# Optimization experiments

Hardware: AMD Instinct MI355X
Metric: run time of the kernel (lower is better)

## Reference

```python
import jax, jax.numpy as jnp
import numpy as np

N = 8192
IN_DIM = 256
OUT_DIM = 256  # out_dim//num_heads * num_heads == out_dim
EDGE_PROB = 0.01


def setup_inputs() -> dict:
    key = jax.random.key(0)
    k_adj, k_h, k_q, k_k, k_v = jax.random.split(key, 5)
    # Dense 0/1 adjacency mask, multiplied into the score matrix.
    adj = (jax.random.uniform(k_adj, (N, N)) < EDGE_PROB).astype(jnp.float32)
    h = jax.random.normal(k_h, (N, IN_DIM), dtype=jnp.float32)
    # torch nn.Linear stores weight as [out_features, in_features]; no bias (use_bias=False).
    s = 1.0 / np.sqrt(IN_DIM)
    Wq = jax.random.normal(k_q, (OUT_DIM, IN_DIM), dtype=jnp.float32) * s
    Wk = jax.random.normal(k_k, (OUT_DIM, IN_DIM), dtype=jnp.float32) * s
    Wv = jax.random.normal(k_v, (OUT_DIM, IN_DIM), dtype=jnp.float32) * s
    return {"adj": adj, "h": h, "Wq": Wq, "Wk": Wk, "Wv": Wv}


def reference(adj, h, Wq, Wk, Wv):
    # Q_h, K_h, V_h: [N, out_dim]
    Q_h = h @ Wq.T
    K_h = h @ Wk.T
    V_h = h @ Wv.T
    scale = 1.0 / jnp.sqrt(jnp.asarray(h.shape[1], dtype=h.dtype))
    # Scores masked multiplicatively by adjacency (faithful to source: zeros,
    # not -inf, so non-edges still contribute exp(0) after softmax).
    A_tilde = scale * (Q_h @ K_h.T) * adj            # [N, N]
    attention = jax.nn.softmax(A_tilde, axis=1)       # softmax over dim 1
    X_tilde = attention @ V_h                         # [N, out_dim]
    return X_tilde
```

## Files before the change

kernel.cpp:

```cpp
#include <hip/hip_runtime.h>


#define NN  8192
#define DIM 256
#define SCALE 0.0625f
#define CAP 128

typedef __attribute__((ext_vector_type(8))) short short8;
typedef __attribute__((ext_vector_type(4))) float f32x4;
typedef __attribute__((ext_vector_type(4))) unsigned int u32x4;

__device__ __forceinline__ unsigned short f2bf(float f) {
    union { float f; unsigned u; } v; v.f = f;
    unsigned u = v.u;
    unsigned r = (u + 0x7fffu + ((u >> 16) & 1u)) >> 16;
    return (unsigned short)r;
}
__device__ __forceinline__ float bf2f(unsigned short s) {
    union { unsigned u; float f; } v; v.u = ((unsigned)s) << 16;
    return v.f;
}
__device__ __forceinline__ float dw_lo(unsigned u) {
    union { unsigned u; float f; } v; v.u = u << 16; return v.f;
}
__device__ __forceinline__ float dw_hi(unsigned u) {
    union { unsigned u; float f; } v; v.u = u & 0xffff0000u; return v.f;
}

__global__ __launch_bounds__(256) void prep_kernel(
    const float* __restrict__ h, const float* __restrict__ Wq,
    const float* __restrict__ Wk, const float* __restrict__ Wv,
    unsigned short* __restrict__ h_bf, unsigned short* __restrict__ w_bf)
{
    int b = blockIdx.x, t = threadIdx.x;
    if (b < 2048) {
        int idx = (b * 256 + t) * 4;
        float4 v = *(const float4*)(h + idx);
        ushort4 o; o.x = f2bf(v.x); o.y = f2bf(v.y); o.z = f2bf(v.z); o.w = f2bf(v.w);
        *(ushort4*)(h_bf + idx) = o;
    } else {
        int idx = ((b - 2048) * 256 + t) * 4;
        int w = idx >> 16;
        int offn = idx & 65535;
        const float* src = (w == 0) ? Wq : (w == 1) ? Wk : Wv;
        float4 v = *(const float4*)(src + offn);
        ushort4 o; o.x = f2bf(v.x); o.y = f2bf(v.y); o.z = f2bf(v.z); o.w = f2bf(v.w);
        *(ushort4*)(w_bf + idx) = o;
    }
}

__global__ __launch_bounds__(256) void proj_gemm(
    const unsigned short* __restrict__ h_bf, const unsigned short* __restrict__ w_bf,
    float* __restrict__ Q, unsigned short* __restrict__ Kb, unsigned short* __restrict__ Vb)
{
    __shared__ unsigned short sB[256][40];
    const int mb = blockIdx.x, p = blockIdx.y;
    const unsigned short* W = w_bf + (p << 16);
    const int tid = threadIdx.x, wave = tid >> 6, lane = tid & 63;

    f32x4 acc[16];
#pragma unroll
    for (int f = 0; f < 16; ++f) acc[f] = (f32x4)(0.0f);

    const int arow = mb * 64 + wave * 16 + (lane & 15);
    const int ko   = (lane >> 4) * 8;

    for (int kk = 0; kk < 256; kk += 32) {
        __syncthreads();
        {
            const uint4* src = (const uint4*)(W + tid * 256 + kk);
            uint4* dst = (uint4*)(&sB[tid][0]);
            dst[0] = src[0]; dst[1] = src[1]; dst[2] = src[2]; dst[3] = src[3];
        }
        __syncthreads();
        short8 a = *(const short8*)(h_bf + (size_t)arow * 256 + kk + ko);
#pragma unroll
        for (int f = 0; f < 16; ++f) {
            short8 b = *(const short8*)(&sB[f * 16 + (lane & 15)][ko]);
            acc[f] = __builtin_amdgcn_mfma_f32_16x16x32_bf16(a, b, acc[f], 0, 0, 0);
        }
    }

    const int orow = mb * 64 + wave * 16 + ((lane >> 4) << 2);
    const int ocol = lane & 15;
    if (p == 0) {
#pragma unroll
        for (int f = 0; f < 16; ++f)
#pragma unroll
            for (int r = 0; r < 4; ++r)
                Q[(size_t)(orow + r) * 256 + f * 16 + ocol] = acc[f][r];
    } else {
        unsigned short* dstb = (p == 1) ? Kb : Vb;
#pragma unroll
        for (int f = 0; f < 16; ++f)
#pragma unroll
            for (int r = 0; r < 4; ++r)
                dstb[(size_t)(orow + r) * 256 + f * 16 + ocol] = f2bf(acc[f][r]);
    }
}

__global__ __launch_bounds__(256) void vsum_partial(
    const unsigned short* __restrict__ Vb, float* __restrict__ partial)
{
    int b = blockIdx.x, t = threadIdx.x;
    float s = 0.0f;
    for (int r = 0; r < 64; ++r)
        s += bf2f(Vb[(size_t)(b * 64 + r) * 256 + t]);
    partial[b * 256 + t] = s;
}
__global__ __launch_bounds__(256) void vsum_final(
    const float* __restrict__ partial, float* __restrict__ Vsum)
{
    int t = threadIdx.x;
    float s = 0.0f;
    for (int b = 0; b < 128; ++b) s += partial[b * 256 + t];
    Vsum[t] = s;
}

__global__ __launch_bounds__(256) void attn_main(
    const float* __restrict__ adj, const float* __restrict__ Q,
    const unsigned short* __restrict__ Kb, const unsigned short* __restrict__ Vb,
    const float* __restrict__ Vsum, float* __restrict__ out)
{
    __shared__ int   s_idx[4][CAP];
    __shared__ float s_acc[4][256];
    __shared__ float s_den[4];

    const int i    = blockIdx.x;
    const int tid  = threadIdx.x;
    const int lane = tid & 63;
    const int wave = tid >> 6;

    const f32x4* arow = (const f32x4*)(adj + (size_t)i * NN);
    f32x4 av[8];
#pragma unroll
    for (int it = 0; it < 8; ++it)
        av[it] = __builtin_nontemporal_load(arow + (wave * 512 + it * 64 + lane));

    const unsigned long long lt = (1ull << lane) - 1ull;
    int off = 0;
#pragma unroll
    for (int it = 0; it < 8; ++it) {
        const int colbase = (wave * 512 + it * 64 + lane) * 4;
#pragma unroll
        for (int c = 0; c < 4; ++c) {
            bool nz = (av[it][c] != 0.0f);
            unsigned long long m = __ballot(nz);
            if (nz) s_idx[wave][off + __popcll(m & lt)] = colbase + c;
            off += __popcll(m);
        }
    }

    const float* Qi = Q + (size_t)i * DIM + (lane & 15) * 16;
    f32x4 q0 = *(const f32x4*)(Qi);
    f32x4 q1 = *(const f32x4*)(Qi + 4);
    f32x4 q2 = *(const f32x4*)(Qi + 8);
    f32x4 q3 = *(const f32x4*)(Qi + 12);

    const int g = lane >> 4;
    float acc0 = 0.f, acc1 = 0.f, acc2 = 0.f, acc3 = 0.f, den = 0.f;
    const int rounds = (off + 3) >> 2;

#pragma unroll 2
    for (int r = 0; r < rounds; ++r) {
        const int kb0 = r * 4;
        int jg0 = (kb0 + 0 < off) ? s_idx[wave][kb0 + 0] : 0;
        int jg1 = (kb0 + 1 < off) ? s_idx[wave][kb0 + 1] : 0;
        int jg2 = (kb0 + 2 < off) ? s_idx[wave][kb0 + 2] : 0;
        int jg3 = (kb0 + 3 < off) ? s_idx[wave][kb0 + 3] : 0;

        const bool myv = (kb0 + g) < off;
        const int  myj = (g == 0) ? jg0 : (g == 1) ? jg1 : (g == 2) ? jg2 : jg3;

        const u32x4* kp = (const u32x4*)(Kb + (size_t)myj * DIM + (lane & 15) * 16);
        u32x4 ka = kp[0];
        u32x4 kc = kp[1];

        ushort4 v0 = *(const ushort4*)(Vb + (size_t)jg0 * DIM + lane * 4);
        ushort4 v1 = *(const ushort4*)(Vb + (size_t)jg1 * DIM + lane * 4);
        ushort4 v2 = *(const ushort4*)(Vb + (size_t)jg2 * DIM + lane * 4);
        ushort4 v3 = *(const ushort4*)(Vb + (size_t)jg3 * DIM + lane * 4);

        float d0 = q0[0] * dw_lo(ka[0]);
        float d1 = q0[1] * dw_hi(ka[0]);
        float d2 = q0[2] * dw_lo(ka[1]);
        float d3 = q0[3] * dw_hi(ka[1]);
        d0 = fmaf(q1[0], dw_lo(ka[2]), d0);
        d1 = fmaf(q1[1], dw_hi(ka[2]), d1);
        d2 = fmaf(q1[2], dw_lo(ka[3]), d2);
        d3 = fmaf(q1[3], dw_hi(ka[3]), d3);
        d0 = fmaf(q2[0], dw_lo(kc[0]), d0);
        d1 = fmaf(q2[1], dw_hi(kc[0]), d1);
        d2 = fmaf(q2[2], dw_lo(kc[1]), d2);
        d3 = fmaf(q2[3], dw_hi(kc[1]), d3);
        d0 = fmaf(q3[0], dw_lo(kc[2]), d0);
        d1 = fmaf(q3[1], dw_hi(kc[2]), d1);
        d2 = fmaf(q3[2], dw_lo(kc[3]), d2);
        d3 = fmaf(q3[3], dw_hi(kc[3]), d3);
        float d = (d0 + d1) + (d2 + d3);

        d += __shfl_xor(d, 1);
        d += __shfl_xor(d, 2);
        d += __shfl_xor(d, 4);
        d += __shfl_xor(d, 8);

        float e = myv ? (__expf(SCALE * d) - 1.0f) : 0.0f;

        float e0 = __shfl(e, 0);
        float e1 = __shfl(e, 16);
        float e2 = __shfl(e, 32);
        float e3 = __shfl(e, 48);
        den += (e0 + e1) + (e2 + e3);

        acc0 = fmaf(e0, bf2f(v0.x), acc0); acc1 = fmaf(e0, bf2f(v0.y), acc1);
        acc2 = fmaf(e0, bf2f(v0.z), acc2); acc3 = fmaf(e0, bf2f(v0.w), acc3);
        acc0 = fmaf(e1, bf2f(v1.x), acc0); acc1 = fmaf(e1, bf2f(v1.y), acc1);
        acc2 = fmaf(e1, bf2f(v1.z), acc2); acc3 = fmaf(e1, bf2f(v1.w), acc3);
        acc0 = fmaf(e2, bf2f(v2.x), acc0); acc1 = fmaf(e2, bf2f(v2.y), acc1);
        acc2 = fmaf(e2, bf2f(v2.z), acc2); acc3 = fmaf(e2, bf2f(v2.w), acc3);
        acc0 = fmaf(e3, bf2f(v3.x), acc0); acc1 = fmaf(e3, bf2f(v3.y), acc1);
        acc2 = fmaf(e3, bf2f(v3.z), acc2); acc3 = fmaf(e3, bf2f(v3.w), acc3);
    }

    f32x4 accv = {acc0, acc1, acc2, acc3};
    *(f32x4*)(&s_acc[wave][lane * 4]) = accv;
    if (lane == 0) s_den[wave] = den;
    __syncthreads();

    float a = (s_acc[0][tid] + s_acc[1][tid]) + (s_acc[2][tid] + s_acc[3][tid]);
    float dn = (s_den[0] + s_den[1]) + (s_den[2] + s_den[3]);
    out[(size_t)i * DIM + tid] = (Vsum[tid] + a) / (8192.0f + dn);
}

extern "C" void kernel_launch(void* const* d_in, const int* in_sizes, int n_in,
                              void* d_out, int out_size, void* d_ws, size_t ws_size,
                              hipStream_t stream)
{
    const float* adj = (const float*)d_in[0];
    const float* h   = (const float*)d_in[1];
    const float* Wq  = (const float*)d_in[2];
    const float* Wk  = (const float*)d_in[3];
    const float* Wv  = (const float*)d_in[4];
    float* out = (float*)d_out;

    char* ws = (char*)d_ws;
    size_t off = 0;
    unsigned short* p_hbf = (unsigned short*)(ws + off); off += (size_t)NN * DIM * 2;
    unsigned short* p_wbf = (unsigned short*)(ws + off); off += (size_t)3 * DIM * DIM * 2;
    off = (off + 1023) & ~(size_t)1023;
    float*          p_Q   = (float*)(ws + off);          off += (size_t)NN * DIM * 4;
    unsigned short* p_Kb  = (unsigned short*)(ws + off); off += (size_t)NN * DIM * 2;
    unsigned short* p_Vb  = (unsigned short*)(ws + off); off += (size_t)NN * DIM * 2;
    float*          p_par = (float*)(ws + off);          off += (size_t)128 * DIM * 4;
    float*          p_vs  = (float*)(ws + off);          off += DIM * 4;
    (void)ws_size; (void)in_sizes; (void)n_in; (void)out_size;

    prep_kernel<<<2240, 256, 0, stream>>>(h, Wq, Wk, Wv, p_hbf, p_wbf);
    proj_gemm<<<dim3(128, 3), 256, 0, stream>>>(p_hbf, p_wbf, p_Q, p_Kb, p_Vb);
    vsum_partial<<<128, 256, 0, stream>>>(p_Vb, p_par);
    vsum_final<<<1, 256, 0, stream>>>(p_par, p_vs);
    attn_main<<<NN, 256, 0, stream>>>(adj, p_Q, p_Kb, p_Vb, p_vs, out);
}
```

Measured before the change: 133.6 us.

## Split attention rows into column chunks with bf16 partials and finalize pass

Attention is restructured so each wave handles one row over a 1024-column slice of the adjacency. That gives 8 partial numerators per row, stored as bf16, plus partial denominators, and a new finalize kernel sums them. The intent is more parallelism and less per-wave serial work, with no cross-wave shared-memory reduction. The cost is an extra launch and extra partial-sum traffic, and bf16 partials lose precision. The per-slice index cap of 32 silently drops edges if a slice ever holds more than 32 nonzeros, which happens in random rows at this edge density (mean about 10 per slice, though exceeding 32 is very unlikely).

```diff
diff --git a/kernel.cpp b/kernel.cpp
--- a/kernel.cpp
+++ b/kernel.cpp
@@ -4,11 +4,12 @@
 #define NN  8192
 #define DIM 256
 #define SCALE 0.0625f
-#define CAP 128
+#define CAP 32
 
 typedef __attribute__((ext_vector_type(8))) short short8;
 typedef __attribute__((ext_vector_type(4))) float f32x4;
 typedef __attribute__((ext_vector_type(4))) unsigned int u32x4;
+typedef __attribute__((ext_vector_type(4))) unsigned short u16x4;
 
 __device__ __forceinline__ unsigned short f2bf(float f) {
     union { float f; unsigned u; } v; v.f = f;
@@ -117,39 +118,24 @@
     Vsum[t] = s;
 }
 
-__global__ __launch_bounds__(256) void attn_main(
+__global__ __launch_bounds__(128) void attn_e(
     const float* __restrict__ adj, const float* __restrict__ Q,
     const unsigned short* __restrict__ Kb, const unsigned short* __restrict__ Vb,
-    const float* __restrict__ Vsum, float* __restrict__ out)
-{
-    __shared__ int   s_idx[4][CAP];
-    __shared__ float s_acc[4][256];
-    __shared__ float s_den[4];
-
-    const int i    = blockIdx.x;
-    const int tid  = threadIdx.x;
-    const int lane = tid & 63;
-    const int wave = tid >> 6;
-
-    const f32x4* arow = (const f32x4*)(adj + (size_t)i * NN);
-    f32x4 av[8];
-#pragma unroll
-    for (int it = 0; it < 8; ++it)
-        av[it] = __builtin_nontemporal_load(arow + (wave * 512 + it * 64 + lane));
-
+    unsigned short* __restrict__ pnum, float* __restrict__ pden)
+{
+    __shared__ unsigned short s_idx[2][CAP];
+
+    const int e    = blockIdx.x >> 12;
+    const int i    = ((blockIdx.x & 4095) << 1) + (threadIdx.x >> 6);
+    const int lane = threadIdx.x & 63;
+    const int w    = threadIdx.x >> 6;
     const unsigned long long lt = (1ull << lane) - 1ull;
-    int off = 0;
-#pragma unroll
-    for (int it = 0; it < 8; ++it) {
-        const int colbase = (wave * 512 + it * 64 + lane) * 4;
-#pragma unroll
-        for (int c = 0; c < 4; ++c) {
-            bool nz = (av[it][c] != 0.0f);
-            unsigned long long m = __ballot(nz);
-            if (nz) s_idx[wave][off + __popcll(m & lt)] = colbase + c;
-            off += __popcll(m);
-        }
-    }
+
+    const f32x4* arow4 = (const f32x4*)(adj + (size_t)i * NN + e * 1024);
+    f32x4 a0 = __builtin_nontemporal_load(arow4 + lane);
+    f32x4 a1 = __builtin_nontemporal_load(arow4 + 64 + lane);
+    f32x4 a2 = __builtin_nontemporal_load(arow4 + 128 + lane);
+    f32x4 a3 = __builtin_nontemporal_load(arow4 + 192 + lane);
 
     const float* Qi = Q + (size_t)i * DIM + (lane & 15) * 16;
     f32x4 q0 = *(const f32x4*)(Qi);
@@ -157,19 +143,38 @@
     f32x4 q2 = *(const f32x4*)(Qi + 8);
     f32x4 q3 = *(const f32x4*)(Qi + 12);
 
+    const int jbase = e * 1024;
+    int off = 0;
+#pragma unroll
+    for (int s = 0; s < 4; ++s) {
+        f32x4 av = (s == 0) ? a0 : (s == 1) ? a1 : (s == 2) ? a2 : a3;
+        const int colbase = jbase + (s * 64 + lane) * 4;
+#pragma unroll
+        for (int c = 0; c < 4; ++c) {
+            bool nz = (av[c] != 0.0f);
+            unsigned long long m = __ballot(nz);
+            if (nz) {
+                int pos = off + __popcll(m & lt);
+                if (pos < CAP) s_idx[w][pos] = (unsigned short)(colbase + c);
+            }
+            off += __popcll(m);
+        }
+    }
+    const int cnt = (off < CAP) ? off : CAP;
+
     const int g = lane >> 4;
     float acc0 = 0.f, acc1 = 0.f, acc2 = 0.f, acc3 = 0.f, den = 0.f;
-    const int rounds = (off + 3) >> 2;
+    const int rounds = (cnt + 3) >> 2;
 
 #pragma unroll 2
     for (int r = 0; r < rounds; ++r) {
         const int kb0 = r * 4;
-        int jg0 = (kb0 + 0 < off) ? s_idx[wave][kb0 + 0] : 0;
-        int jg1 = (kb0 + 1 < off) ? s_idx[wave][kb0 + 1] : 0;
-        int jg2 = (kb0 + 2 < off) ? s_idx[wave][kb0 + 2] : 0;
-        int jg3 = (kb0 + 3 < off) ? s_idx[wave][kb0 + 3] : 0;
-
-        const bool myv = (kb0 + g) < off;
+        int jg0 = (kb0 + 0 < cnt) ? (int)s_idx[w][kb0 + 0] : 0;
+        int jg1 = (kb0 + 1 < cnt) ? (int)s_idx[w][kb0 + 1] : 0;
+        int jg2 = (kb0 + 2 < cnt) ? (int)s_idx[w][kb0 + 2] : 0;
+        int jg3 = (kb0 + 3 < cnt) ? (int)s_idx[w][kb0 + 3] : 0;
+
+        const bool myv = (kb0 + g) < cnt;
         const int  myj = (g == 0) ? jg0 : (g == 1) ? jg1 : (g == 2) ? jg2 : jg3;
 
         const u32x4* kp = (const u32x4*)(Kb + (size_t)myj * DIM + (lane & 15) * 16);
@@ -204,12 +209,12 @@
         d += __shfl_xor(d, 4);
         d += __shfl_xor(d, 8);
 
-        float e = myv ? (__expf(SCALE * d) - 1.0f) : 0.0f;
-
-        float e0 = __shfl(e, 0);
-        float e1 = __shfl(e, 16);
-        float e2 = __shfl(e, 32);
-        float e3 = __shfl(e, 48);
+        float ev = myv ? (__expf(SCALE * d) - 1.0f) : 0.0f;
+
+        float e0 = __shfl(ev, 0);
+        float e1 = __shfl(ev, 16);
+        float e2 = __shfl(ev, 32);
+        float e3 = __shfl(ev, 48);
         den += (e0 + e1) + (e2 + e3);
 
         acc0 = fmaf(e0, bf2f(v0.x), acc0); acc1 = fmaf(e0, bf2f(v0.y), acc1);
@@ -222,14 +227,23 @@
         acc2 = fmaf(e3, bf2f(v3.z), acc2); acc3 = fmaf(e3, bf2f(v3.w), acc3);
     }
 
-    f32x4 accv = {acc0, acc1, acc2, acc3};
-    *(f32x4*)(&s_acc[wave][lane * 4]) = accv;
-    if (lane == 0) s_den[wave] = den;
-    __syncthreads();
-
-    float a = (s_acc[0][tid] + s_acc[1][tid]) + (s_acc[2][tid] + s_acc[3][tid]);
-    float dn = (s_den[0] + s_den[1]) + (s_den[2] + s_den[3]);
-    out[(size_t)i * DIM + tid] = (Vsum[tid] + a) / (8192.0f + dn);
+    u16x4 o = { f2bf(acc0), f2bf(acc1), f2bf(acc2), f2bf(acc3) };
+    __builtin_nontemporal_store(o, (u16x4*)(pnum + ((size_t)i * 8 + e) * 256 + lane * 4));
+    if (lane == 0) pden[(size_t)i * 8 + e] = den;
+}
+
+__global__ __launch_bounds__(256) void finalize(
+    const unsigned short* __restrict__ pnum, const float* __restrict__ pden,
+    const float* __restrict__ Vsum, float* __restrict__ out)
+{
+    const int i = blockIdx.x, t = threadIdx.x;
+    float num = 0.0f, den = 0.0f;
+#pragma unroll
+    for (int x = 0; x < 8; ++x) {
+        num += bf2f(pnum[((size_t)i * 8 + x) * 256 + t]);
+        den += pden[(size_t)i * 8 + x];
+    }
+    out[(size_t)i * DIM + t] = (Vsum[t] + num) / (8192.0f + den);
 }
 
 extern "C" void kernel_launch(void* const* d_in, const int* in_sizes, int n_in,
@@ -253,11 +267,14 @@
     unsigned short* p_Vb  = (unsigned short*)(ws + off); off += (size_t)NN * DIM * 2;
     float*          p_par = (float*)(ws + off);          off += (size_t)128 * DIM * 4;
     float*          p_vs  = (float*)(ws + off);          off += DIM * 4;
+    unsigned short* p_pn  = (unsigned short*)(ws + off); off += (size_t)NN * 8 * 256 * 2;
+    float*          p_pd  = (float*)(ws + off);          off += (size_t)NN * 8 * 4;
     (void)ws_size; (void)in_sizes; (void)n_in; (void)out_size;
 
     prep_kernel<<<2240, 256, 0, stream>>>(h, Wq, Wk, Wv, p_hbf, p_wbf);
     proj_gemm<<<dim3(128, 3), 256, 0, stream>>>(p_hbf, p_wbf, p_Q, p_Kb, p_Vb);
     vsum_partial<<<128, 256, 0, stream>>>(p_Vb, p_par);
     vsum_final<<<1, 256, 0, stream>>>(p_par, p_vs);
-    attn_main<<<NN, 256, 0, stream>>>(adj, p_Q, p_Kb, p_Vb, p_vs, out);
-}
+    attn_e<<<NN * 8 / 2, 128, 0, stream>>>(adj, p_Q, p_Kb, p_Vb, p_pn, p_pd);
+    finalize<<<NN, 256, 0, stream>>>(p_pn, p_pd, p_vs, out);
+}
```

Measured after the change: 131.8 us. Within noise of the previous version (-1.3%).
